# Optimization experiments

Measured on AMD Instinct MI355X. Metric: run time of the kernel, lower is better.

The kernel has to match this reference:

```python
import jax, jax.numpy as jnp
import numpy as np

N = 64
DX0 = np.pi / N
B = 4096
N_ENV = 8
CODE = 128


def setup_inputs() -> dict:
    key = jax.random.key(0)
    k1, k2, k3 = jax.random.split(key, 3)
    y0 = jax.random.normal(k1, (B, 1, N, N), dtype=jnp.float32)
    env = jax.random.randint(k2, (B,), 0, N_ENV).astype(jnp.int64)
    codes = jax.random.normal(k3, (B, CODE), dtype=jnp.float32)
    t = jnp.zeros((1,), dtype=jnp.float32)
    # learned params: [mu, domain_placeholder] per env (matches nn.Parameter init)
    params = jnp.concatenate([jnp.full((N_ENV, 1), 0.005, jnp.float32),
                              jnp.full((N_ENV, 1), 1.0, jnp.float32)], axis=1)
    # fixed domain buffer for n_env == 8
    domain = jnp.array([0.75, 1.0, 0.75, 1.0, 0.75, 1.0, 0.75, 1.0],
                       dtype=jnp.float32)[:, None]  # [n_env, 1]
    return {"t": t, "y0": y0, "env": env, "codes": codes,
            "params": params, "domain": domain}


def _dx(a):  # roll along last axis (torch dims=2 on [B,H,W])
    return jnp.roll(a, -1, axis=2) - jnp.roll(a, 1, axis=2)


def _dy(a):  # roll along axis 1
    return jnp.roll(a, -1, axis=1) - jnp.roll(a, 1, axis=1)


def _laplacian2d(a, fdx2):
    # torch conv2d (cross-correlation) with kernel [[0,1,0],[1,-4,1],[1,1,0]]
    # and circular padding; note the asymmetric bottom row (faithful to source).
    lap = (jnp.roll(a, 1, axis=1)                    # a[i-1, j]
           + jnp.roll(a, 1, axis=2)                  # a[i, j-1]
           - 4.0 * a
           + jnp.roll(a, -1, axis=2)                 # a[i, j+1]
           + jnp.roll(jnp.roll(a, -1, axis=1), 1, axis=2)  # a[i+1, j-1]
           + jnp.roll(a, -1, axis=1))                # a[i+1, j]
    return lap / fdx2


def _poisson_solve(w, fdx):
    # w: [B,N,N]; fdx: [B,1] grid spacing per sample
    w_pad = jnp.pad(w, ((0, 0), (0, 1), (0, 1)), mode='wrap')  # [B,N+1,N+1]
    wf = jnp.fft.fft2(w_pad / (N ** 2))
    base = jnp.fft.fftfreq(N + 1).astype(w.dtype)       # fftfreq(n, d) = base / d
    k = (2.0 * np.pi) * base[None, :] / fdx             # [B, N+1]
    k2 = k[:, :, None] ** 2 + k[:, None, :] ** 2        # [B, N+1, N+1]
    uf = -wf / (1e-12 + k2)
    uf = uf.at[:, 0, 0].set(0.0)
    return jnp.fft.ifft2((N ** 2) * uf).real[:, :N, :N]


def reference(t, y0, env, codes, params, domain):
    x = y0[:, 0]                              # [B,N,N]
    p = params[env]                           # [B,2]
    mu = p[:, 0:1][..., None]                 # [B,1,1]
    fdx = domain[env] * DX0                   # [B,1]
    psi = _poisson_solve(-x, fdx)             # [B,N,N]
    fdx2 = (fdx[..., None]) ** 2              # [B,1,1]

    rxm = jnp.roll(x, -1, axis=2); rxp = jnp.roll(x, 1, axis=2)
    rym = jnp.roll(x, -1, axis=1); ryp = jnp.roll(x, 1, axis=1)
    pxm = jnp.roll(psi, -1, axis=2); pxp = jnp.roll(psi, 1, axis=2)
    pym = jnp.roll(psi, -1, axis=1); pyp = jnp.roll(psi, 1, axis=1)

    J1 = (_dy(psi) * _dx(x) - _dx(psi) * _dy(x)) / (4.0 * fdx2)
    J2 = (rxm * _dy(pxm) - rxp * _dy(pxp)
          - rym * _dx(pym) + ryp * _dx(pyp)) / (4.0 * fdx2)
    J3 = (jnp.roll(rxm, -1, axis=1) * (pym - pxm)
          - jnp.roll(rxp, 1, axis=1) * (pxp - pyp)
          - jnp.roll(rxp, -1, axis=1) * (pym - pxp)
          + jnp.roll(rxm, 1, axis=1) * (pxm - pyp)) / (4.0 * fdx2)

    dudt = -(J1 + J2 + J3) / 3.0 + mu * _laplacian2d(x, fdx2)
    return dudt[:, None]                      # [B,1,N,N]
```

## Files before the change

### kernel.cpp

```cpp
#include <hip/hip_runtime.h>
#include <math.h>


typedef _Float16 half8 __attribute__((ext_vector_type(8)));
typedef _Float16 half4 __attribute__((ext_vector_type(4)));
typedef float floatx4 __attribute__((ext_vector_type(4)));

#define WPI 0.09666439165562847f

#define H_TB1 0
#define H_TA2 10240
#define H_TG  20480
#define H_TH  26624
#define F_GR32 16384
#define F_GI32 16432
#define F_HC32 16480
#define F_HS32 16528
#define F_SE   16576

__device__ __forceinline__ float trig65(int t, int isSin) {
    return isSin ? sinf(WPI * (float)t) : cosf(WPI * (float)t);
}

__global__ void setup_tables(float* __restrict__ ws, const float* __restrict__ domain) {
    int idx = blockIdx.x * 256 + threadIdx.x;
    _Float16* tbH = (_Float16*)ws;
    const float inv = 1.0f / 4225.0f;
    if (idx < 32768) {
        float v = 0.0f;
        int part;
        if (idx < 10240) {
            int chunk = idx >> 9, within = idx & 511;
            part = chunk & 1; int kc = (chunk >> 1) & 1, ni = chunk >> 2;
            int l2 = within >> 3, j = within & 7;
            int row = 16 * ni + (l2 & 15);
            int k = 32 * kc + 8 * (l2 >> 4) + j;
            if (row < 66) {
                int c = (row < 32) ? row : (row < 64 ? row - 32 : 32);
                int isS = (row < 32) ? 0 : (row < 64 ? 1 : row - 64);
                v = trig65((k * c) % 65, isS);
                if (k == 0) v += trig65((64 * c) % 65, isS);
            }
        } else if (idx < 20480) {
            int i2 = idx - 10240;
            int chunk = i2 >> 9, within = i2 & 511;
            part = chunk & 1; int kc = (chunk >> 1) & 1, mi = chunk >> 2;
            int l2 = within >> 3, j = within & 7;
            int row = 16 * mi + (l2 & 15);
            int m = 32 * kc + 8 * (l2 >> 4) + j;
            if (row < 66) {
                int jr = (row < 32) ? row : (row < 64 ? row - 32 : 32);
                int isS = (row < 32) ? 0 : (row < 64 ? 1 : row - 64);
                float s = isS ? 1.0f : -1.0f;
                v = s * trig65((jr * m) % 65, isS);
                if (m == 0) v += s * trig65((jr * 64) % 65, isS);
            }
        } else if (idx < 26624) {
            int i2 = idx - 20480;
            int chunk = i2 >> 9, within = i2 & 511;
            part = chunk & 1; int g = (chunk >> 1) & 1, si = chunk >> 2;
            int l2 = within >> 3, j = within & 7;
            int s = 16 * si + (l2 & 15);
            int jj = 8 * (l2 >> 4) + j;
            if (s <= 32) v = trig65((s * jj) % 65, g);
        } else {
            int i2 = idx - 26624;
            int chunk = i2 >> 9, within = i2 & 511;
            part = chunk & 1; int h = (chunk >> 1) & 1, pi2 = chunk >> 2;
            int l2 = within >> 3, j = within & 7;
            int p = 16 * pi2 + (l2 & 15);
            int c = 8 * (l2 >> 4) + j;
            if (p <= 32) {
                if (c == 0) v = h ? 0.0f : inv;
                else v = 2.0f * inv * trig65((c * p) % 65, h);
            }
        }
        _Float16 hh = (_Float16)v;
        tbH[idx] = part ? (_Float16)(v - (float)hh) : hh;
    } else if (idx < 32960) {
        int i2 = idx - 32768;
        int grp = i2 / 48, s = i2 - grp * 48;
        float v = 0.0f;
        if (s <= 32) {
            int t = (32 * s) % 65;
            float cs = cosf(WPI * t), sn = sinf(WPI * t);
            v = (grp == 0) ? cs : (grp == 1) ? sn : (grp == 2) ? 2.0f * inv * cs : 2.0f * inv * sn;
        }
        ws[F_GR32 + i2] = v;
    } else if (idx < 41672) {
        int i2 = idx - 32960;
        int e2 = i2 / 1089, rem = i2 - e2 * 1089;
        int a = rem / 33, b2 = rem - a * 33;
        const float DX0 = 0.04908738521234052f;
        float fdx = domain[e2] * DX0;
        float tt = 6.283185307179586f / (65.0f * fdx);
        float s2v = tt * tt;
        ws[F_SE + i2] = -1.0f / (1e-12f + s2v * (float)(a * a + b2 * b2));
    }
}

#define MFMA16(A, B, C) __builtin_amdgcn_mfma_f32_16x16x32_f16((A), (B), (C), 0, 0, 0)

__global__ __launch_bounds__(256, 4)
void turb_kernel(const float* __restrict__ y0, const int* __restrict__ env,
                 const float* __restrict__ params, const float* __restrict__ domain,
                 const float* __restrict__ ws, float* __restrict__ out) {
    __shared__ __align__(16) char lds_raw[40448];
    _Float16* Yt  = (_Float16*)lds_raw;
    _Float16* Xr  = (_Float16*)lds_raw;
    _Float16* Xi  = (_Float16*)(lds_raw + 9216);
    float*    X32r = (float*)(lds_raw + 18432);
    float*    X32i = (float*)(lds_raw + 18688);
    _Float16* ST  = (_Float16*)(lds_raw + 18944);
    float*    S32 = (float*)(lds_raw + 18944 + 19008);
    float*    psiT = (float*)(lds_raw + 18944);

    const int b = blockIdx.x, tid = threadIdx.x;
    const int wid = tid >> 6, lane = tid & 63, n16 = lane & 15, q = lane >> 4;
    const int e = env[b];
    const _Float16* tbH = (const _Float16*)ws;
    const float* tf = ws;
    const float* Se = tf + F_SE + e * 1089;
    const float* x0 = y0 + (size_t)b * 4096;

    {
        half8 Ah[2], Al[2];
        const float* xrow = x0 + (16 * wid + n16) * 64 + 8 * q;
        #pragma unroll
        for (int kc = 0; kc < 2; kc++) {
            float4 v0 = *(const float4*)(xrow + 32 * kc);
            float4 v1 = *(const float4*)(xrow + 32 * kc + 4);
            float vv[8] = {v0.x, v0.y, v0.z, v0.w, v1.x, v1.y, v1.z, v1.w};
            #pragma unroll
            for (int u = 0; u < 8; u++) {
                _Float16 h = (_Float16)vv[u];
                Ah[kc][u] = h; Al[kc][u] = (_Float16)(vv[u] - (float)h);
            }
        }
        for (int ni = 0; ni < 5; ni++) {
            floatx4 acc = {0.f, 0.f, 0.f, 0.f};
            #pragma unroll
            for (int kc = 0; kc < 2; kc++) {
                half8 Bh = *(const half8*)(tbH + H_TB1 + ((ni * 2 + kc) * 2 + 0) * 512 + lane * 8);
                half8 Bl = *(const half8*)(tbH + H_TB1 + ((ni * 2 + kc) * 2 + 1) * 512 + lane * 8);
                acc = MFMA16(Ah[kc], Bh, acc);
                acc = MFMA16(Ah[kc], Bl, acc);
                acc = MFMA16(Al[kc], Bh, acc);
            }
            int cp = 16 * ni + n16;
            if (ni < 4 || n16 < 2) {
                half4 hh, ll;
                #pragma unroll
                for (int i = 0; i < 4; i++) {
                    _Float16 h = (_Float16)acc[i];
                    hh[i] = h; ll[i] = (_Float16)(acc[i] - (float)h);
                }
                *(half4*)(Yt + cp * 136 + 16 * wid + 4 * q) = hh;
                *(half4*)(Yt + cp * 136 + 64 + 16 * wid + 4 * q) = ll;
            }
        }
    }
    __syncthreads();

    for (int pos = wid; pos < 25; pos += 4) {
        int mi = pos / 5, ni = pos - 5 * mi;
        floatx4 acc = {0.f, 0.f, 0.f, 0.f};
        #pragma unroll
        for (int kc = 0; kc < 2; kc++) {
            half8 Ah = *(const half8*)(tbH + H_TA2 + ((mi * 2 + kc) * 2 + 0) * 512 + lane * 8);
            half8 Al = *(const half8*)(tbH + H_TA2 + ((mi * 2 + kc) * 2 + 1) * 512 + lane * 8);
            half8 Bh = *(const half8*)(Yt + (16 * ni + n16) * 136 + 32 * kc + 8 * q);
            half8 Bl = *(const half8*)(Yt + (16 * ni + n16) * 136 + 64 + 32 * kc + 8 * q);
            acc = MFMA16(Ah, Bh, acc);
            acc = MFMA16(Ah, Bl, acc);
            acc = MFMA16(Al, Bh, acc);
        }
        if ((ni < 4) || (n16 < 2)) {
            int cp = 16 * ni + n16;
            int cc = (ni == 4) ? 32 : (cp & 31);
            int isS = (ni == 4) ? n16 : (ni >> 1);
            if (mi < 4) {
                int isQ = mi >> 1;
                int sid = isQ ? (isS ? 3 : 1) : (isS ? 2 : 0);
                int jjb = 16 * (mi & 1) + 4 * q;
                half4 hh, ll;
                #pragma unroll
                for (int i = 0; i < 4; i++) {
                    float S = Se[cc * 33 + jjb + i];
                    float v = 2.0f * S * acc[i];
                    if (sid == 2) v = -v;
                    _Float16 h = (_Float16)v;
                    hh[i] = h; ll[i] = (_Float16)(v - (float)h);
                }
                _Float16* sb = ST + sid * 2376 + cc * 72 + jjb;
                *(half4*)sb = hh;
                *(half4*)(sb + 32) = ll;
            } else if (q == 0) {
                float S = Se[cc * 33 + 32];
                #pragma unroll
                for (int i = 0; i < 2; i++) {
                    int sid = i ? (isS ? 3 : 1) : (isS ? 2 : 0);
                    float v = 2.0f * S * acc[i];
                    if (sid == 2) v = -v;
                    S32[sid * 33 + cc] = v;
                }
            }
        }
    }
    __syncthreads();

    if (tid < 33) {
        int c = tid;
        float v0[4];
        #pragma unroll
        for (int sid = 0; sid < 4; sid++)
            v0[sid] = (float)ST[sid * 2376 + c * 72] + (float)ST[sid * 2376 + c * 72 + 32];
        float pr = 0.5f * (v0[0] + v0[3]), pi = 0.5f * (v0[1] + v0[2]);
        if (c == 0) { pr = 0.f; pi = 0.f; }
        float outs[4] = {pr, pi, pi, pr};
        #pragma unroll
        for (int sid = 0; sid < 4; sid++) {
            _Float16 h = (_Float16)outs[sid];
            ST[sid * 2376 + c * 72] = h;
            ST[sid * 2376 + c * 72 + 32] = (_Float16)(outs[sid] - (float)h);
        }
    }
    __syncthreads();

    for (int pos = wid; pos < 9; pos += 4) {
        int ci = pos / 3, si = pos - 3 * ci;
        int arow = (16 * ci + n16) * 72 + 8 * q;
        half8 A0h = *(const half8*)(ST + arow),           A0l = *(const half8*)(ST + arow + 32);
        half8 A1h = *(const half8*)(ST + 2376 + arow),    A1l = *(const half8*)(ST + 2376 + arow + 32);
        half8 A2h = *(const half8*)(ST + 4752 + arow),    A2l = *(const half8*)(ST + 4752 + arow + 32);
        half8 A3h = *(const half8*)(ST + 7128 + arow),    A3l = *(const half8*)(ST + 7128 + arow + 32);
        half8 Grh = *(const half8*)(tbH + H_TG + ((si * 2 + 0) * 2 + 0) * 512 + lane * 8);
        half8 Grl = *(const half8*)(tbH + H_TG + ((si * 2 + 0) * 2 + 1) * 512 + lane * 8);
        half8 Gih = *(const half8*)(tbH + H_TG + ((si * 2 + 1) * 2 + 0) * 512 + lane * 8);
        half8 Gil = *(const half8*)(tbH + H_TG + ((si * 2 + 1) * 2 + 1) * 512 + lane * 8);
        floatx4 aA = {0.f,0.f,0.f,0.f}, aB = aA, aC = aA, aD = aA;
        aA = MFMA16(A0h, Grh, aA); aA = MFMA16(A0h, Grl, aA); aA = MFMA16(A0l, Grh, aA);
        aB = MFMA16(A1h, Gih, aB); aB = MFMA16(A1h, Gil, aB); aB = MFMA16(A1l, Gih, aB);
        aC = MFMA16(A2h, Grh, aC); aC = MFMA16(A2h, Grl, aC); aC = MFMA16(A2l, Grh, aC);
        aD = MFMA16(A3h, Gih, aD); aD = MFMA16(A3h, Gil, aD); aD = MFMA16(A3l, Gih, aD);
        int s = 16 * si + n16;
        float ga = tf[F_GR32 + s], gi2 = tf[F_GI32 + s];
        bool sval = (si < 2) || (n16 == 0);
        if (ci < 2) {
            half4 hP, lP, hQ, lQ, hM, lM, hN, lN;
            #pragma unroll
            for (int i = 0; i < 4; i++) {
                int c = 16 * ci + 4 * q + i;
                float u0 = S32[c], u1 = S32[33 + c], u2 = S32[66 + c], u3 = S32[99 + c];
                float av = aA[i] + ga * u0, bv = aB[i] + gi2 * u1;
                float cv = aC[i] + ga * u2, dv = aD[i] + gi2 * u3;
                float xrP = av - bv, xiP = cv + dv, xrM = av + bv, xiM = cv - dv;
                _Float16 h;
                h = (_Float16)xrP; hP[i] = h; lP[i] = (_Float16)(xrP - (float)h);
                h = (_Float16)xiP; hQ[i] = h; lQ[i] = (_Float16)(xiP - (float)h);
                h = (_Float16)xrM; hM[i] = h; lM[i] = (_Float16)(xrM - (float)h);
                h = (_Float16)xiM; hN[i] = h; lN[i] = (_Float16)(xiM - (float)h);
            }
            int cb = 16 * ci + 4 * q;
            if (sval) {
                *(half4*)(Xr + s * 72 + cb) = hP;  *(half4*)(Xr + s * 72 + 32 + cb) = lP;
                *(half4*)(Xi + s * 72 + cb) = hQ;  *(half4*)(Xi + s * 72 + 32 + cb) = lQ;
                if (s >= 2) {
                    int sm = 65 - s;
                    *(half4*)(Xr + sm * 72 + cb) = hM;  *(half4*)(Xr + sm * 72 + 32 + cb) = lM;
                    *(half4*)(Xi + sm * 72 + cb) = hN;  *(half4*)(Xi + sm * 72 + 32 + cb) = lN;
                }
            }
        } else if (q == 0 && sval) {
            float u0 = S32[32], u1 = S32[65], u2 = S32[98], u3 = S32[131];
            float av = aA[0] + ga * u0, bv = aB[0] + gi2 * u1;
            float cv = aC[0] + ga * u2, dv = aD[0] + gi2 * u3;
            X32r[s] = av - bv; X32i[s] = cv + dv;
            if (s >= 2) { X32r[65 - s] = av + bv; X32i[65 - s] = cv - dv; }
        }
    }
    __syncthreads();

    for (int pos = wid; pos < 12; pos += 4) {
        int ri = pos / 3, pti = pos - 3 * ri;
        int brow = (16 * ri + n16) * 72 + 8 * q;
        half8 Brh = *(const half8*)(Xr + brow), Brl = *(const half8*)(Xr + brow + 32);
        half8 Bih = *(const half8*)(Xi + brow), Bil = *(const half8*)(Xi + brow + 32);
        half8 Hch = *(const half8*)(tbH + H_TH + ((pti * 2 + 0) * 2 + 0) * 512 + lane * 8);
        half8 Hcl = *(const half8*)(tbH + H_TH + ((pti * 2 + 0) * 2 + 1) * 512 + lane * 8);
        half8 Hsh = *(const half8*)(tbH + H_TH + ((pti * 2 + 1) * 2 + 0) * 512 + lane * 8);
        half8 Hsl = *(const half8*)(tbH + H_TH + ((pti * 2 + 1) * 2 + 1) * 512 + lane * 8);
        floatx4 aE = {0.f,0.f,0.f,0.f}, aF = aE;
        aE = MFMA16(Hch, Brh, aE); aE = MFMA16(Hch, Brl, aE); aE = MFMA16(Hcl, Brh, aE);
        aF = MFMA16(Hsh, Bih, aF); aF = MFMA16(Hsh, Bil, aF); aF = MFMA16(Hsl, Bih, aF);
        int r = 16 * ri + n16;
        float xr32 = X32r[r], xi32 = X32i[r];
        #pragma unroll
        for (int i = 0; i < 4; i++) {
            int p = 16 * pti + 4 * q + i;
            if (pti < 2 || (q == 0 && i == 0)) {
                float E = aE[i] + xr32 * tf[F_HC32 + p];
                float F = aF[i] + xi32 * tf[F_HS32 + p];
                psiT[p * 65 + r] = E - F;
                if (p >= 2) psiT[(65 - p) * 65 + r] = E + F;
            }
        }
    }
    __syncthreads();

    {
        const int c = lane;
        const int cm1 = (c + 63) & 63, cp1 = (c + 1) & 63;
        const float mu = params[2 * e];
        const float DX0 = 0.04908738521234052f;
        const float fdx = domain[e] * DX0;
        const float fdx2 = fdx * fdx;
        const float inv12 = 1.0f / (12.0f * fdx2);
        const float invf = mu / fdx2;
        float* o = out + (size_t)b * 4096;
        const int r0 = wid * 16;
        int rm = (r0 + 63) & 63;
        float xLm = x0[rm * 64 + cm1], xCm = x0[rm * 64 + c], xRm = x0[rm * 64 + cp1];
        float pLm = psiT[cm1 * 65 + rm], pCm = psiT[c * 65 + rm], pRm = psiT[cp1 * 65 + rm];
        float xLc = x0[r0 * 64 + cm1], xCc = x0[r0 * 64 + c], xRc = x0[r0 * 64 + cp1];
        float pLc = psiT[cm1 * 65 + r0], pCc = psiT[c * 65 + r0], pRc = psiT[cp1 * 65 + r0];
        #pragma unroll
        for (int it = 0; it < 16; it++) {
            int r = r0 + it;
            int rn = (r + 1) & 63;
            float xLp = x0[rn * 64 + cm1], xCp = x0[rn * 64 + c], xRp = x0[rn * 64 + cp1];
            float pLp = psiT[cm1 * 65 + rn], pCp = psiT[c * 65 + rn], pRp = psiT[cp1 * 65 + rn];
            float J1 = (pCp - pCm) * (xRc - xLc) - (pRc - pLc) * (xCp - xCm);
            float J2 = xRc * (pRp - pRm) - xLc * (pLp - pLm) - xCp * (pRp - pLp) + xCm * (pRm - pLm);
            float J3 = xRp * (pCp - pRc) - xLm * (pLc - pCm) - xLp * (pCp - pLc) + xRm * (pRc - pCm);
            float lap = xCm + xLc - 4.f * xCc + xRc + xLp + xCp;
            o[r * 64 + c] = -(J1 + J2 + J3) * inv12 + lap * invf;
            xLm = xLc; xCm = xCc; xRm = xRc; pLm = pLc; pCm = pCc; pRm = pRc;
            xLc = xLp; xCc = xCp; xRc = xRp; pLc = pLp; pCc = pCp; pRc = pRp;
        }
    }
}

extern "C" void kernel_launch(void* const* d_in, const int* in_sizes, int n_in,
                              void* d_out, int out_size, void* d_ws, size_t ws_size,
                              hipStream_t stream) {
    const float* y0     = (const float*)d_in[1];
    const int*   env    = (const int*)d_in[2];
    const float* params = (const float*)d_in[4];
    const float* domain = (const float*)d_in[5];
    float* out = (float*)d_out;
    float* ws  = (float*)d_ws;

    setup_tables<<<dim3(163), dim3(256), 0, stream>>>(ws, domain);
    turb_kernel<<<dim3(4096), dim3(256), 0, stream>>>(y0, env, params, domain, ws, out);
}
```

Baseline: 182.7 us.

## Double block to 512 threads and split each DFT stage across eight waves

After: 187.5 us. 1.03x slower.

```diff
diff --git a/kernel.cpp b/kernel.cpp
--- a/kernel.cpp
+++ b/kernel.cpp
@@ -101,7 +101,7 @@
 
 #define MFMA16(A, B, C) __builtin_amdgcn_mfma_f32_16x16x32_f16((A), (B), (C), 0, 0, 0)
 
-__global__ __launch_bounds__(256, 4)
+__global__ __launch_bounds__(512, 8)
 void turb_kernel(const float* __restrict__ y0, const int* __restrict__ env,
                  const float* __restrict__ params, const float* __restrict__ domain,
                  const float* __restrict__ ws, float* __restrict__ out) {
@@ -124,8 +124,9 @@
     const float* x0 = y0 + (size_t)b * 4096;
 
     {
+        const int mi = wid & 3;
         half8 Ah[2], Al[2];
-        const float* xrow = x0 + (16 * wid + n16) * 64 + 8 * q;
+        const float* xrow = x0 + (16 * mi + n16) * 64 + 8 * q;
         #pragma unroll
         for (int kc = 0; kc < 2; kc++) {
             float4 v0 = *(const float4*)(xrow + 32 * kc);
@@ -137,7 +138,9 @@
                 Ah[kc][u] = h; Al[kc][u] = (_Float16)(vv[u] - (float)h);
             }
         }
-        for (int ni = 0; ni < 5; ni++) {
+        const int niBeg = (wid & 4) ? 3 : 0;
+        const int niEnd = (wid & 4) ? 5 : 3;
+        for (int ni = niBeg; ni < niEnd; ni++) {
             floatx4 acc = {0.f, 0.f, 0.f, 0.f};
             #pragma unroll
             for (int kc = 0; kc < 2; kc++) {
@@ -155,14 +158,14 @@
                     _Float16 h = (_Float16)acc[i];
                     hh[i] = h; ll[i] = (_Float16)(acc[i] - (float)h);
                 }
-                *(half4*)(Yt + cp * 136 + 16 * wid + 4 * q) = hh;
-                *(half4*)(Yt + cp * 136 + 64 + 16 * wid + 4 * q) = ll;
-            }
-        }
-    }
-    __syncthreads();
-
-    for (int pos = wid; pos < 25; pos += 4) {
+                *(half4*)(Yt + cp * 136 + 16 * mi + 4 * q) = hh;
+                *(half4*)(Yt + cp * 136 + 64 + 16 * mi + 4 * q) = ll;
+            }
+        }
+    }
+    __syncthreads();
+
+    for (int pos = wid; pos < 25; pos += 8) {
         int mi = pos / 5, ni = pos - 5 * mi;
         floatx4 acc = {0.f, 0.f, 0.f, 0.f};
         #pragma unroll
@@ -227,61 +230,57 @@
     }
     __syncthreads();
 
-    for (int pos = wid; pos < 9; pos += 4) {
-        int ci = pos / 3, si = pos - 3 * ci;
+    for (int pos = wid; pos < 18; pos += 8) {
+        int ci = pos / 6, rem = pos - 6 * ci;
+        int si = rem >> 1, g = rem & 1;
         int arow = (16 * ci + n16) * 72 + 8 * q;
-        half8 A0h = *(const half8*)(ST + arow),           A0l = *(const half8*)(ST + arow + 32);
-        half8 A1h = *(const half8*)(ST + 2376 + arow),    A1l = *(const half8*)(ST + 2376 + arow + 32);
-        half8 A2h = *(const half8*)(ST + 4752 + arow),    A2l = *(const half8*)(ST + 4752 + arow + 32);
-        half8 A3h = *(const half8*)(ST + 7128 + arow),    A3l = *(const half8*)(ST + 7128 + arow + 32);
+        const _Float16* st0 = ST + (2 * g) * 2376;
+        half8 A0h = *(const half8*)(st0 + arow),        A0l = *(const half8*)(st0 + arow + 32);
+        half8 A1h = *(const half8*)(st0 + 2376 + arow), A1l = *(const half8*)(st0 + 2376 + arow + 32);
         half8 Grh = *(const half8*)(tbH + H_TG + ((si * 2 + 0) * 2 + 0) * 512 + lane * 8);
         half8 Grl = *(const half8*)(tbH + H_TG + ((si * 2 + 0) * 2 + 1) * 512 + lane * 8);
         half8 Gih = *(const half8*)(tbH + H_TG + ((si * 2 + 1) * 2 + 0) * 512 + lane * 8);
         half8 Gil = *(const half8*)(tbH + H_TG + ((si * 2 + 1) * 2 + 1) * 512 + lane * 8);
-        floatx4 aA = {0.f,0.f,0.f,0.f}, aB = aA, aC = aA, aD = aA;
+        floatx4 aA = {0.f,0.f,0.f,0.f}, aB = aA;
         aA = MFMA16(A0h, Grh, aA); aA = MFMA16(A0h, Grl, aA); aA = MFMA16(A0l, Grh, aA);
         aB = MFMA16(A1h, Gih, aB); aB = MFMA16(A1h, Gil, aB); aB = MFMA16(A1l, Gih, aB);
-        aC = MFMA16(A2h, Grh, aC); aC = MFMA16(A2h, Grl, aC); aC = MFMA16(A2l, Grh, aC);
-        aD = MFMA16(A3h, Gih, aD); aD = MFMA16(A3h, Gil, aD); aD = MFMA16(A3l, Gih, aD);
         int s = 16 * si + n16;
         float ga = tf[F_GR32 + s], gi2 = tf[F_GI32 + s];
         bool sval = (si < 2) || (n16 == 0);
+        _Float16* Xo = g ? Xi : Xr;
+        float* X32o = g ? X32i : X32r;
+        const float sgn = g ? 1.0f : -1.0f;
         if (ci < 2) {
-            half4 hP, lP, hQ, lQ, hM, lM, hN, lN;
+            half4 hP, lP, hM, lM;
             #pragma unroll
             for (int i = 0; i < 4; i++) {
                 int c = 16 * ci + 4 * q + i;
-                float u0 = S32[c], u1 = S32[33 + c], u2 = S32[66 + c], u3 = S32[99 + c];
+                float u0 = S32[(2 * g) * 33 + c], u1 = S32[(2 * g + 1) * 33 + c];
                 float av = aA[i] + ga * u0, bv = aB[i] + gi2 * u1;
-                float cv = aC[i] + ga * u2, dv = aD[i] + gi2 * u3;
-                float xrP = av - bv, xiP = cv + dv, xrM = av + bv, xiM = cv - dv;
+                float xP = av + sgn * bv;
+                float xM = av - sgn * bv;
                 _Float16 h;
-                h = (_Float16)xrP; hP[i] = h; lP[i] = (_Float16)(xrP - (float)h);
-                h = (_Float16)xiP; hQ[i] = h; lQ[i] = (_Float16)(xiP - (float)h);
-                h = (_Float16)xrM; hM[i] = h; lM[i] = (_Float16)(xrM - (float)h);
-                h = (_Float16)xiM; hN[i] = h; lN[i] = (_Float16)(xiM - (float)h);
+                h = (_Float16)xP; hP[i] = h; lP[i] = (_Float16)(xP - (float)h);
+                h = (_Float16)xM; hM[i] = h; lM[i] = (_Float16)(xM - (float)h);
             }
             int cb = 16 * ci + 4 * q;
             if (sval) {
-                *(half4*)(Xr + s * 72 + cb) = hP;  *(half4*)(Xr + s * 72 + 32 + cb) = lP;
-                *(half4*)(Xi + s * 72 + cb) = hQ;  *(half4*)(Xi + s * 72 + 32 + cb) = lQ;
+                *(half4*)(Xo + s * 72 + cb) = hP;  *(half4*)(Xo + s * 72 + 32 + cb) = lP;
                 if (s >= 2) {
                     int sm = 65 - s;
-                    *(half4*)(Xr + sm * 72 + cb) = hM;  *(half4*)(Xr + sm * 72 + 32 + cb) = lM;
-                    *(half4*)(Xi + sm * 72 + cb) = hN;  *(half4*)(Xi + sm * 72 + 32 + cb) = lN;
+                    *(half4*)(Xo + sm * 72 + cb) = hM;  *(half4*)(Xo + sm * 72 + 32 + cb) = lM;
                 }
             }
         } else if (q == 0 && sval) {
-            float u0 = S32[32], u1 = S32[65], u2 = S32[98], u3 = S32[131];
+            float u0 = S32[(2 * g) * 33 + 32], u1 = S32[(2 * g + 1) * 33 + 32];
             float av = aA[0] + ga * u0, bv = aB[0] + gi2 * u1;
-            float cv = aC[0] + ga * u2, dv = aD[0] + gi2 * u3;
-            X32r[s] = av - bv; X32i[s] = cv + dv;
-            if (s >= 2) { X32r[65 - s] = av + bv; X32i[65 - s] = cv - dv; }
-        }
-    }
-    __syncthreads();
-
-    for (int pos = wid; pos < 12; pos += 4) {
+            X32o[s] = av + sgn * bv;
+            if (s >= 2) X32o[65 - s] = av - sgn * bv;
+        }
+    }
+    __syncthreads();
+
+    for (int pos = wid; pos < 12; pos += 8) {
         int ri = pos / 3, pti = pos - 3 * ri;
         int brow = (16 * ri + n16) * 72 + 8 * q;
         half8 Brh = *(const half8*)(Xr + brow), Brl = *(const half8*)(Xr + brow + 32);
@@ -318,14 +317,14 @@
         const float inv12 = 1.0f / (12.0f * fdx2);
         const float invf = mu / fdx2;
         float* o = out + (size_t)b * 4096;
-        const int r0 = wid * 16;
+        const int r0 = wid * 8;
         int rm = (r0 + 63) & 63;
         float xLm = x0[rm * 64 + cm1], xCm = x0[rm * 64 + c], xRm = x0[rm * 64 + cp1];
         float pLm = psiT[cm1 * 65 + rm], pCm = psiT[c * 65 + rm], pRm = psiT[cp1 * 65 + rm];
         float xLc = x0[r0 * 64 + cm1], xCc = x0[r0 * 64 + c], xRc = x0[r0 * 64 + cp1];
         float pLc = psiT[cm1 * 65 + r0], pCc = psiT[c * 65 + r0], pRc = psiT[cp1 * 65 + r0];
         #pragma unroll
-        for (int it = 0; it < 16; it++) {
+        for (int it = 0; it < 8; it++) {
             int r = r0 + it;
             int rn = (r + 1) & 63;
             float xLp = x0[rn * 64 + cm1], xCp = x0[rn * 64 + c], xRp = x0[rn * 64 + cp1];
@@ -352,5 +351,5 @@
     float* ws  = (float*)d_ws;
 
     setup_tables<<<dim3(163), dim3(256), 0, stream>>>(ws, domain);
-    turb_kernel<<<dim3(4096), dim3(256), 0, stream>>>(y0, env, params, domain, ws, out);
+    turb_kernel<<<dim3(4096), dim3(512), 0, stream>>>(y0, env, params, domain, ws, out);
 }
```
